# Performance work log

Measured on AMD Instinct MI355X. Metric: run time of the kernel, lower is better.

## Reference

```python
import jax, jax.numpy as jnp
import numpy as np

SENSOR_DIM = 256
MODEL_DIM = 512
NUM_DATASETS = 8


def setup_inputs() -> dict:
    key = jax.random.key(0)
    k1, k2, k3 = jax.random.split(key, 3)
    x = jax.random.normal(k1, (32, 200, 1024), dtype=jnp.float32)
    dataset_id = jax.random.randint(k2, (32,), 0, NUM_DATASETS)
    # Conv1d weight [out_ch, in_ch, k] and bias, as in torch.nn.Conv1d
    W = jax.random.normal(k3, (NUM_DATASETS * MODEL_DIM, SENSOR_DIM, 3), dtype=jnp.float32) * 0.02
    b = jnp.zeros((NUM_DATASETS * MODEL_DIM,), dtype=jnp.float32)
    return {"x": x, "dataset_id": dataset_id, "W": W, "b": b}


def reference(x, dataset_id, W, b):
    B, c_in, T = x.shape
    # DatasetPadding: zero-pad channel dim up to sensor_dim
    if c_in < SENSOR_DIM:
        x = jnp.pad(x, ((0, 0), (0, SENSOR_DIM - c_in), (0, 0)))
    # Conv1d(sensor_dim -> num_datasets*model_dim, kernel=3, padding=1)
    y = jax.lax.conv_general_dilated(
        x, W, window_strides=(1,), padding=((1, 1),),
        dimension_numbers=("NCH", "OIH", "NCH"))
    y = y + b[None, :, None]
    y = jax.nn.gelu(y, approximate=False)  # torch GELU default = exact erf
    # unflatten channels to (num_datasets, model_dim) and select per-example dataset slice
    y = y.reshape(B, NUM_DATASETS, MODEL_DIM, T)
    onehot = jax.nn.one_hot(dataset_id, NUM_DATASETS, dtype=y.dtype)  # [B, D]
    out = jnp.einsum("bdmt,bd->bmt", y, onehot)  # [B, model_dim, T]
    return out
```

## Files before the change

### kernel.cpp

```cpp
#include <hip/hip_runtime.h>


typedef unsigned short u16;
typedef __attribute__((ext_vector_type(8))) short bf16x8;
typedef __attribute__((ext_vector_type(4))) float f32x4;

#define CIN 200
#define CINP 224
#define T 1024
#define BATCH 32
#define MD 512
#define XT_ROWS 1026
#define NCHUNK 7
#define XP_PITCH 202
#define TT 256
#define XROWS (TT + 2)
#define XGRAN (XROWS * 4)
#define WOB 256
#define WF_PER_OB (21 * 512)

__device__ __forceinline__ u16 f2bf(float f) {
    unsigned u = __float_as_uint(f);
    u += 0x7FFFu + ((u >> 16) & 1u);
    return (u16)(u >> 16);
}

__device__ __forceinline__ void g2l16(void* lds, const void* g) {
    __builtin_amdgcn_global_load_lds(
        (const __attribute__((address_space(1))) unsigned int*)(uintptr_t)g,
        (__attribute__((address_space(3))) unsigned int*)(unsigned)(uintptr_t)lds,
        16, 0, 0);
}

__global__ __launch_bounds__(256) void prep(const float* __restrict__ x,
                                            const float* __restrict__ W,
                                            u16* __restrict__ xt,
                                            u16* __restrict__ wf) {
    __shared__ __align__(16) unsigned char smem[16 * 673 * 4];
    const int tid = threadIdx.x;
    if (blockIdx.x < 512) {
        u16* tile = (u16*)smem;
        const int b  = blockIdx.x >> 4;
        const int bx = blockIdx.x & 15;
        const int t0 = bx * 64;
        const int tl = tid & 63;
        const int w  = tid >> 6;
        const float* xb = x + (size_t)b * CIN * T + t0 + tl;
        for (int i = w; i < CIN; i += 4)
            tile[tl * XP_PITCH + i] = f2bf(xb[(size_t)i * T]);
        __syncthreads();
        u16* xrow = xt + ((size_t)b * XT_ROWS + 1 + t0) * CINP;
        for (int it = 0; it < 16; ++it) {
            int r = it * 4 + w;
            if (tl < 56) {
                ushort4 v = {0, 0, 0, 0};
                if (tl < 50) {
                    const u16* p = tile + r * XP_PITCH + tl * 4;
                    v.x = p[0]; v.y = p[1]; v.z = p[2]; v.w = p[3];
                }
                *(ushort4*)(xrow + (size_t)r * CINP + tl * 4) = v;
            }
        }
        if (bx == 0 && tid < 112)
            ((unsigned*)(xt + (size_t)b * XT_ROWS * CINP))[tid] = 0;
        if (bx == 15 && tid < 112)
            ((unsigned*)(xt + ((size_t)b * XT_ROWS + 1025) * CINP))[tid] = 0;
    } else {
        float* wtile = (float*)smem;
        const int ob = blockIdx.x - 512;
        const float* wp = W + (size_t)ob * 16 * 768;
        for (int j = tid; j < 16 * 672; j += 256) {
            int o = j / 672, r = j - o * 672;
            wtile[o * 673 + r] = wp[(size_t)o * 768 + r];
        }
        __syncthreads();
        u16* wo = wf + (size_t)ob * WF_PER_OB;
        for (int j = tid; j < WF_PER_OB; j += 256) {
            int e    = j & 7;
            int lane = (j >> 3) & 63;
            int kc   = j >> 9;
            int cc   = kc % 7, k = kc / 7;
            int l = lane & 15, q = lane >> 4;
            int i = cc * 32 + q * 8 + e;
            wo[j] = f2bf(wtile[l * 673 + i * 3 + k]);
        }
    }
}

__global__ __launch_bounds__(256, 2) void conv_mfma(const u16* __restrict__ xt,
                                                    const u16* __restrict__ wf,
                                                    const int* __restrict__ dsid,
                                                    const float* __restrict__ bias,
                                                    float* __restrict__ out) {
    __shared__ __align__(16) u16 xs[2 * XGRAN * 8];

    const int tid = threadIdx.x;
    const int wave = tid >> 6, lane = tid & 63;
    const int l = lane & 15, quad = lane >> 4;
    const int wm  = (wave & 1) * 64;
    const int wti = (wave >> 1) * 128;

    const int id  = blockIdx.x;
    const int xcd = id & 7;
    const int j   = id >> 3;
    const int b   = xcd * 4 + (j >> 4);
    const int m0  = ((j >> 2) & 3) * 128;
    const int t0  = (j & 3) * TT;
    const int d  = dsid[b];
    const int obase = d * MD + m0;

    f32x4 acc[4][8];
#pragma unroll
    for (int mi = 0; mi < 4; ++mi)
#pragma unroll
        for (int ti = 0; ti < 8; ++ti) acc[mi][ti] = (f32x4){0.f, 0.f, 0.f, 0.f};

    const u16* xbase = xt + ((size_t)b * XT_ROWS + t0) * CINP;
    const u16* wfw = wf + (size_t)((obase + wm) >> 4) * WF_PER_OB + lane * 8;

    const u16* xsrc[5]; u16* xdst[5];
#pragma unroll
    for (int k = 0; k < 5; ++k) {
        int g = tid + k * 256;
        int r = g >> 2, p = g & 3, s = p ^ ((r >> 1) & 3);
        if (g < XGRAN) { xsrc[k] = xbase + (size_t)r * CINP + s * 8; xdst[k] = xs + (size_t)(g & ~63) * 8; }
        else           { xsrc[k] = xbase;                            xdst[k] = xs; }
    }

    auto stage = [&](int bsel, int c) {
        const int ic  = c * 32;
        const int off = bsel * (XGRAN * 8);
#pragma unroll
        for (int k = 0; k < 5; ++k)
            if (tid + k * 256 < XGRAN) g2l16(xdst[k] + off, xsrc[k] + ic);
    };
    auto loadw = [&](bf16x8* dst, int tap, int c) {
#pragma unroll
        for (int mi = 0; mi < 4; ++mi)
            dst[mi] = *(const bf16x8*)(wfw + (size_t)((mi * 21 + tap * 7 + c) << 9));
    };

    bf16x8 acur[4], w1[4], w2[4];
    stage(0, 0);
    loadw(acur, 0, 0);
    __syncthreads();

#pragma unroll
    for (int c = 0; c < NCHUNK; ++c) {
        const u16* xb = xs + (c & 1) * (XGRAN * 8);
        loadw(w1, 1, c);
        loadw(w2, 2, c);
        if (c + 1 < NCHUNK) stage((c & 1) ^ 1, c + 1);

#pragma unroll
        for (int tap = 0; tap < 3; ++tap) {
            const bf16x8* af = (tap == 0) ? acur : (tap == 1) ? w1 : w2;
            if (tap == 2 && c + 1 < NCHUNK) loadw(acur, 0, c + 1);
#pragma unroll
            for (int ti = 0; ti < 8; ++ti) {
                int row = wti + tap + ti * 16 + l;
                bf16x8 bv = *(const bf16x8*)(xb + ((size_t)row * 4 + (quad ^ ((row >> 1) & 3))) * 8);
                __builtin_amdgcn_s_setprio(1);
#pragma unroll
                for (int mi = 0; mi < 4; ++mi)
                    acc[mi][ti] = __builtin_amdgcn_mfma_f32_16x16x32_bf16(af[mi], bv, acc[mi][ti], 0, 0, 0);
                __builtin_amdgcn_s_setprio(0);
            }
        }

        if (c + 1 < NCHUNK) {
            asm volatile("s_waitcnt vmcnt(4)" ::: "memory");
            __builtin_amdgcn_s_barrier();
            __builtin_amdgcn_sched_barrier(0);
        }
    }

#pragma unroll
    for (int mi = 0; mi < 4; ++mi) {
        float bvv[4];
#pragma unroll
        for (int r = 0; r < 4; ++r)
            bvv[r] = bias[obase + wm + mi * 16 + quad * 4 + r];
#pragma unroll
        for (int ti = 0; ti < 8; ++ti) {
            int t = t0 + wti + ti * 16 + l;
#pragma unroll
            for (int r = 0; r < 4; ++r) {
                int m = wm + mi * 16 + quad * 4 + r;
                float v = acc[mi][ti][r] + bvv[r];
                float p2 = v * v;
                float z2 = v * fmaf(p2, -0.10295089f, -2.30243665f);
                float e = __builtin_amdgcn_exp2f(z2);
                float g = v * __builtin_amdgcn_rcpf(1.0f + e);
                out[((size_t)(b * MD + m0 + m)) * T + t] = g;
            }
        }
    }
}

extern "C" void kernel_launch(void* const* d_in, const int* in_sizes, int n_in,
                              void* d_out, int out_size, void* d_ws, size_t ws_size,
                              hipStream_t stream) {
    const float* x    = (const float*)d_in[0];
    const int*   dsid = (const int*)d_in[1];
    const float* W    = (const float*)d_in[2];
    const float* bias = (const float*)d_in[3];
    float* out = (float*)d_out;

    u16* xt = (u16*)d_ws;
    u16* wf = xt + (size_t)BATCH * XT_ROWS * CINP;

    prep<<<512 + WOB, 256, 0, stream>>>(x, W, xt, wf);
    conv_mfma<<<512, 256, 0, stream>>>(xt, wf, dsid, bias, out);
}
```

Before: 123.1 us.

## Split time tile into halves and stage weight fragments through LDS

The conv kernel now processes its 256-step time tile in two 128-row halves, with half the accumulators per wave, and runs the GELU epilogue for the first half mid-kernel. Weight fragments are no longer loaded per wave from global into registers. They are staged into double-buffered LDS with global_load_lds and read back from there. The aim is to cut register pressure and global weight traffic and to overlap the first epilogue with later compute. In exchange, weights are re-staged for each half, there are more full barriers, and LDS use grows.

```diff
diff --git a/kernel.cpp b/kernel.cpp
--- a/kernel.cpp
+++ b/kernel.cpp
@@ -14,8 +14,9 @@
 #define NCHUNK 7
 #define XP_PITCH 202
 #define TT 256
-#define XROWS (TT + 2)
-#define XGRAN (XROWS * 4)
+#define HROWS 130
+#define XG_H (HROWS * 4)
+#define WFRAGS 24
 #define WOB 256
 #define WF_PER_OB (21 * 512)
 
@@ -92,13 +93,14 @@
                                                     const int* __restrict__ dsid,
                                                     const float* __restrict__ bias,
                                                     float* __restrict__ out) {
-    __shared__ __align__(16) u16 xs[2 * XGRAN * 8];
+    __shared__ __align__(16) u16 xs[2 * XG_H * 8];
+    __shared__ __align__(16) u16 wsm[2 * WFRAGS * 512];
 
     const int tid = threadIdx.x;
     const int wave = tid >> 6, lane = tid & 63;
     const int l = lane & 15, quad = lane >> 4;
     const int wm  = (wave & 1) * 64;
-    const int wti = (wave >> 1) * 128;
+    const int wti = (wave >> 1) * 64;
 
     const int id  = blockIdx.x;
     const int xcd = id & 7;
@@ -109,93 +111,118 @@
     const int d  = dsid[b];
     const int obase = d * MD + m0;
 
-    f32x4 acc[4][8];
+    f32x4 acc[4][4];
 #pragma unroll
     for (int mi = 0; mi < 4; ++mi)
 #pragma unroll
-        for (int ti = 0; ti < 8; ++ti) acc[mi][ti] = (f32x4){0.f, 0.f, 0.f, 0.f};
+        for (int ti = 0; ti < 4; ++ti) acc[mi][ti] = (f32x4){0.f, 0.f, 0.f, 0.f};
 
     const u16* xbase = xt + ((size_t)b * XT_ROWS + t0) * CINP;
-    const u16* wfw = wf + (size_t)((obase + wm) >> 4) * WF_PER_OB + lane * 8;
-
-    const u16* xsrc[5]; u16* xdst[5];
-#pragma unroll
-    for (int k = 0; k < 5; ++k) {
+    const u16* wfb0  = wf + (size_t)((obase) >> 4) * WF_PER_OB + lane * 8;
+    const u16* wfb64 = wf + (size_t)((obase + 64) >> 4) * WF_PER_OB + lane * 8;
+
+    const u16* xsrc[3]; unsigned xdof[3];
+#pragma unroll
+    for (int k = 0; k < 3; ++k) {
         int g = tid + k * 256;
         int r = g >> 2, p = g & 3, s = p ^ ((r >> 1) & 3);
-        if (g < XGRAN) { xsrc[k] = xbase + (size_t)r * CINP + s * 8; xdst[k] = xs + (size_t)(g & ~63) * 8; }
-        else           { xsrc[k] = xbase;                            xdst[k] = xs; }
+        if (g < XG_H) { xsrc[k] = xbase + (size_t)r * CINP + s * 8; xdof[k] = (g & ~63) * 8; }
+        else          { xsrc[k] = xbase;                            xdof[k] = 0; }
     }
 
-    auto stage = [&](int bsel, int c) {
-        const int ic  = c * 32;
-        const int off = bsel * (XGRAN * 8);
-#pragma unroll
-        for (int k = 0; k < 5; ++k)
-            if (tid + k * 256 < XGRAN) g2l16(xdst[k] + off, xsrc[k] + ic);
+    auto stageX = [&](int bsel, int h, int c) {
+        const int adv = h * 128 * CINP + c * 32;
+        u16* base = xs + bsel * (XG_H * 8);
+        g2l16(base + xdof[0], xsrc[0] + adv);
+        g2l16(base + xdof[1], xsrc[1] + adv);
+        if (tid + 512 < XG_H) g2l16(base + xdof[2], xsrc[2] + adv);
     };
-    auto loadw = [&](bf16x8* dst, int tap, int c) {
+    auto stageW = [&](int bsel, int c) {
+#pragma unroll
+        for (int j2 = 0; j2 < 6; ++j2) {
+            int f   = wave * 6 + j2;
+            int rr  = (f >= 12) ? f - 12 : f;
+            int mi  = rr >> 2 ? (rr / 3) : (rr / 3);
+            int tap = rr - mi * 3;
+            const u16* src = ((f >= 12) ? wfb64 : wfb0) + ((mi * 21 + tap * 7 + c) << 9);
+            g2l16(wsm + bsel * (WFRAGS * 512) + f * 512, src);
+        }
+    };
+
+    float bvv[4][4];
+#pragma unroll
+    for (int mi = 0; mi < 4; ++mi)
+#pragma unroll
+        for (int r = 0; r < 4; ++r)
+            bvv[mi][r] = bias[obase + wm + mi * 16 + quad * 4 + r];
+
+    auto epi = [&](int h) {
 #pragma unroll
         for (int mi = 0; mi < 4; ++mi)
-            dst[mi] = *(const bf16x8*)(wfw + (size_t)((mi * 21 + tap * 7 + c) << 9));
+#pragma unroll
+            for (int ti = 0; ti < 4; ++ti) {
+                int t = t0 + h * 128 + wti + ti * 16 + l;
+#pragma unroll
+                for (int r = 0; r < 4; ++r) {
+                    int m = wm + mi * 16 + quad * 4 + r;
+                    float v = acc[mi][ti][r] + bvv[mi][r];
+                    float p2 = v * v;
+                    float z2 = v * fmaf(p2, -0.10295089f, -2.30243665f);
+                    float e = __builtin_amdgcn_exp2f(z2);
+                    float g = v * __builtin_amdgcn_rcpf(1.0f + e);
+                    out[((size_t)(b * MD + m0 + m)) * T + t] = g;
+                }
+            }
     };
 
-    bf16x8 acur[4], w1[4], w2[4];
-    stage(0, 0);
-    loadw(acur, 0, 0);
+    stageX(0, 0, 0); stageW(0, 0);
     __syncthreads();
 
 #pragma unroll
-    for (int c = 0; c < NCHUNK; ++c) {
-        const u16* xb = xs + (c & 1) * (XGRAN * 8);
-        loadw(w1, 1, c);
-        loadw(w2, 2, c);
-        if (c + 1 < NCHUNK) stage((c & 1) ^ 1, c + 1);
-
-#pragma unroll
-        for (int tap = 0; tap < 3; ++tap) {
-            const bf16x8* af = (tap == 0) ? acur : (tap == 1) ? w1 : w2;
-            if (tap == 2 && c + 1 < NCHUNK) loadw(acur, 0, c + 1);
-#pragma unroll
-            for (int ti = 0; ti < 8; ++ti) {
-                int row = wti + tap + ti * 16 + l;
-                bf16x8 bv = *(const bf16x8*)(xb + ((size_t)row * 4 + (quad ^ ((row >> 1) & 3))) * 8);
-                __builtin_amdgcn_s_setprio(1);
+    for (int h = 0; h < 2; ++h) {
+#pragma unroll
+        for (int c = 0; c < NCHUNK; ++c) {
+            const int cc   = h * NCHUNK + c;
+            const int bsel = cc & 1;
+            if (cc == NCHUNK) {
+                epi(0);
 #pragma unroll
                 for (int mi = 0; mi < 4; ++mi)
-                    acc[mi][ti] = __builtin_amdgcn_mfma_f32_16x16x32_bf16(af[mi], bv, acc[mi][ti], 0, 0, 0);
-                __builtin_amdgcn_s_setprio(0);
-            }
-        }
-
-        if (c + 1 < NCHUNK) {
-            asm volatile("s_waitcnt vmcnt(4)" ::: "memory");
-            __builtin_amdgcn_s_barrier();
-            __builtin_amdgcn_sched_barrier(0);
+#pragma unroll
+                    for (int ti = 0; ti < 4; ++ti) acc[mi][ti] = (f32x4){0.f, 0.f, 0.f, 0.f};
+            }
+            if (cc + 1 < 2 * NCHUNK) {
+                const int h2 = (c == NCHUNK - 1) ? h + 1 : h;
+                const int c2 = (c == NCHUNK - 1) ? 0 : c + 1;
+                stageX(bsel ^ 1, h2, c2);
+                stageW(bsel ^ 1, c2);
+            }
+            bf16x8 wfr[4][3];
+            const u16* wb = wsm + bsel * (WFRAGS * 512) + (wm ? 12 * 512 : 0) + lane * 8;
+#pragma unroll
+            for (int mi = 0; mi < 4; ++mi)
+#pragma unroll
+                for (int tap = 0; tap < 3; ++tap)
+                    wfr[mi][tap] = *(const bf16x8*)(wb + (mi * 3 + tap) * 512);
+
+            const u16* xb = xs + bsel * (XG_H * 8);
+#pragma unroll
+            for (int tap = 0; tap < 3; ++tap) {
+#pragma unroll
+                for (int ti = 0; ti < 4; ++ti) {
+                    int row = wti + tap + ti * 16 + l;
+                    bf16x8 bv = *(const bf16x8*)(xb + ((size_t)row * 4 + (quad ^ ((row >> 1) & 3))) * 8);
+                    __builtin_amdgcn_s_setprio(1);
+#pragma unroll
+                    for (int mi = 0; mi < 4; ++mi)
+                        acc[mi][ti] = __builtin_amdgcn_mfma_f32_16x16x32_bf16(wfr[mi][tap], bv, acc[mi][ti], 0, 0, 0);
+                    __builtin_amdgcn_s_setprio(0);
+                }
+            }
+            if (cc + 1 < 2 * NCHUNK) __syncthreads();
         }
     }
-
-#pragma unroll
-    for (int mi = 0; mi < 4; ++mi) {
-        float bvv[4];
-#pragma unroll
-        for (int r = 0; r < 4; ++r)
-            bvv[r] = bias[obase + wm + mi * 16 + quad * 4 + r];
-#pragma unroll
-        for (int ti = 0; ti < 8; ++ti) {
-            int t = t0 + wti + ti * 16 + l;
-#pragma unroll
-            for (int r = 0; r < 4; ++r) {
-                int m = wm + mi * 16 + quad * 4 + r;
-                float v = acc[mi][ti][r] + bvv[r];
-                float p2 = v * v;
-                float z2 = v * fmaf(p2, -0.10295089f, -2.30243665f);
-                float e = __builtin_amdgcn_exp2f(z2);
-                float g = v * __builtin_amdgcn_rcpf(1.0f + e);
-                out[((size_t)(b * MD + m0 + m)) * T + t] = g;
-            }
-        }
-    }
+    epi(1);
 }
 
 extern "C" void kernel_launch(void* const* d_in, const int* in_sizes, int n_in,
```

New measurement: 125.9 us. +2.3%, slower.

## Read input operand directly from global memory instead of staging through LDS

Applied to the files above, without the earlier changes.

Removes the double-buffered LDS staging of the transposed input, along with its barriers and the software-pipelined weight prefetch. Each wave now loads its B fragments directly from global/L2 and loads all three taps' weights at the start of each chunk. This drops the LDS traffic and the block-level synchronization. In exchange it exposes global-load latency without explicit prefetch, and each block re-reads overlapping rows from cache instead of sharing one staged copy.

```diff
diff --git a/kernel.cpp b/kernel.cpp
--- a/kernel.cpp
+++ b/kernel.cpp
@@ -14,8 +14,6 @@
 #define NCHUNK 7
 #define XP_PITCH 202
 #define TT 256
-#define XROWS (TT + 2)
-#define XGRAN (XROWS * 4)
 #define WOB 256
 #define WF_PER_OB (21 * 512)
 
@@ -23,13 +21,6 @@
     unsigned u = __float_as_uint(f);
     u += 0x7FFFu + ((u >> 16) & 1u);
     return (u16)(u >> 16);
-}
-
-__device__ __forceinline__ void g2l16(void* lds, const void* g) {
-    __builtin_amdgcn_global_load_lds(
-        (const __attribute__((address_space(1))) unsigned int*)(uintptr_t)g,
-        (__attribute__((address_space(3))) unsigned int*)(unsigned)(uintptr_t)lds,
-        16, 0, 0);
 }
 
 __global__ __launch_bounds__(256) void prep(const float* __restrict__ x,
@@ -92,8 +83,6 @@
                                                     const int* __restrict__ dsid,
                                                     const float* __restrict__ bias,
                                                     float* __restrict__ out) {
-    __shared__ __align__(16) u16 xs[2 * XGRAN * 8];
-
     const int tid = threadIdx.x;
     const int wave = tid >> 6, lane = tid & 63;
     const int l = lane & 15, quad = lane >> 4;
@@ -115,63 +104,29 @@
 #pragma unroll
         for (int ti = 0; ti < 8; ++ti) acc[mi][ti] = (f32x4){0.f, 0.f, 0.f, 0.f};
 
-    const u16* xbase = xt + ((size_t)b * XT_ROWS + t0) * CINP;
+    const u16* xpl = xt + ((size_t)b * XT_ROWS + t0 + wti + l) * CINP + quad * 8;
     const u16* wfw = wf + (size_t)((obase + wm) >> 4) * WF_PER_OB + lane * 8;
-
-    const u16* xsrc[5]; u16* xdst[5];
-#pragma unroll
-    for (int k = 0; k < 5; ++k) {
-        int g = tid + k * 256;
-        int r = g >> 2, p = g & 3, s = p ^ ((r >> 1) & 3);
-        if (g < XGRAN) { xsrc[k] = xbase + (size_t)r * CINP + s * 8; xdst[k] = xs + (size_t)(g & ~63) * 8; }
-        else           { xsrc[k] = xbase;                            xdst[k] = xs; }
-    }
-
-    auto stage = [&](int bsel, int c) {
-        const int ic  = c * 32;
-        const int off = bsel * (XGRAN * 8);
-#pragma unroll
-        for (int k = 0; k < 5; ++k)
-            if (tid + k * 256 < XGRAN) g2l16(xdst[k] + off, xsrc[k] + ic);
-    };
-    auto loadw = [&](bf16x8* dst, int tap, int c) {
-#pragma unroll
-        for (int mi = 0; mi < 4; ++mi)
-            dst[mi] = *(const bf16x8*)(wfw + (size_t)((mi * 21 + tap * 7 + c) << 9));
-    };
-
-    bf16x8 acur[4], w1[4], w2[4];
-    stage(0, 0);
-    loadw(acur, 0, 0);
-    __syncthreads();
 
 #pragma unroll
     for (int c = 0; c < NCHUNK; ++c) {
-        const u16* xb = xs + (c & 1) * (XGRAN * 8);
-        loadw(w1, 1, c);
-        loadw(w2, 2, c);
-        if (c + 1 < NCHUNK) stage((c & 1) ^ 1, c + 1);
+        bf16x8 wt[3][4];
+#pragma unroll
+        for (int tap = 0; tap < 3; ++tap)
+#pragma unroll
+            for (int mi = 0; mi < 4; ++mi)
+                wt[tap][mi] = *(const bf16x8*)(wfw + (size_t)((mi * 21 + tap * 7 + c) << 9));
 
 #pragma unroll
         for (int tap = 0; tap < 3; ++tap) {
-            const bf16x8* af = (tap == 0) ? acur : (tap == 1) ? w1 : w2;
-            if (tap == 2 && c + 1 < NCHUNK) loadw(acur, 0, c + 1);
 #pragma unroll
             for (int ti = 0; ti < 8; ++ti) {
-                int row = wti + tap + ti * 16 + l;
-                bf16x8 bv = *(const bf16x8*)(xb + ((size_t)row * 4 + (quad ^ ((row >> 1) & 3))) * 8);
+                bf16x8 bv = *(const bf16x8*)(xpl + (size_t)(tap + ti * 16) * CINP + c * 32);
                 __builtin_amdgcn_s_setprio(1);
 #pragma unroll
                 for (int mi = 0; mi < 4; ++mi)
-                    acc[mi][ti] = __builtin_amdgcn_mfma_f32_16x16x32_bf16(af[mi], bv, acc[mi][ti], 0, 0, 0);
+                    acc[mi][ti] = __builtin_amdgcn_mfma_f32_16x16x32_bf16(wt[tap][mi], bv, acc[mi][ti], 0, 0, 0);
                 __builtin_amdgcn_s_setprio(0);
             }
-        }
-
-        if (c + 1 < NCHUNK) {
-            asm volatile("s_waitcnt vmcnt(4)" ::: "memory");
-            __builtin_amdgcn_s_barrier();
-            __builtin_amdgcn_sched_barrier(0);
         }
     }
 
```

Result: slower. 143.0 us (+16.2%).
